# Kernel tuning notes

Measured on AMD Instinct MI355X. Metric: run time of the kernel, lower is better.

Reference implementation:

```python
import jax, jax.numpy as jnp
import numpy as np

D = 1024      # d_model
H = 16        # nhead
HD = D // H   # head_dim = 64
R = HD        # rotary_dim (default = head_dim)
N, T = 2, 2048
W_LEFT, W_RIGHT = 127, 128  # attn_window
ROPE_BASE = 10000.0


def _rope(x, cos, sin):
    # x: [N, T, H, HD]; cos/sin: [1, T, 1, R//2]; non-interleaved (rotate-half)
    x1 = x[..., : R // 2]
    x2 = x[..., R // 2 : R]
    rot = jnp.concatenate([x1 * cos - x2 * sin, x2 * cos + x1 * sin], axis=-1)
    if R < x.shape[-1]:
        rot = jnp.concatenate([rot, x[..., R:]], axis=-1)
    return rot


def setup_inputs() -> dict:
    key = jax.random.key(0)
    k1, k2, k3, k4 = jax.random.split(key, 4)
    x = jax.random.normal(k1, (N, T, D), dtype=jnp.float32)
    w_qkv = jax.random.normal(k2, (3 * D, D), dtype=jnp.float32) * 0.02
    w_out = jax.random.normal(k3, (D, D), dtype=jnp.float32) * 0.02
    b_out = jax.random.normal(k4, (D,), dtype=jnp.float32) * 0.02
    return {"x": x, "w_qkv": w_qkv, "w_out": w_out, "b_out": b_out}


def reference(x, w_qkv, w_out, b_out):
    n, t, _ = x.shape
    qkv = (x @ w_qkv.T).reshape(n, t, 3, H, HD)
    q, k, v = qkv[:, :, 0], qkv[:, :, 1], qkv[:, :, 2]  # [N, T, H, HD]

    # Rotary embedding (flash-attn RotaryEmbedding, interleaved=False)
    pos = jnp.arange(t, dtype=jnp.float32)
    inv_freq = 1.0 / (ROPE_BASE ** (jnp.arange(0, R, 2, dtype=jnp.float32) / R))
    freqs = pos[:, None] * inv_freq[None, :]          # [T, R//2]
    cos = jnp.cos(freqs)[None, :, None, :]
    sin = jnp.sin(freqs)[None, :, None, :]
    q = _rope(q, cos, sin)
    k = _rope(k, cos, sin)

    # Sliding-window band mask: keep j in [i - W_LEFT, i + W_RIGHT]
    i = jnp.arange(t)[:, None]
    j = jnp.arange(t)[None, :]
    band = (j >= i - W_LEFT) & (j <= i + W_RIGHT)      # [T, T] bool
    bias = jnp.where(band, 0.0, -jnp.inf).astype(x.dtype)

    scale = np.float32(1.0 / np.sqrt(HD))
    scores = jnp.einsum('nthd,nshd->nhts', q, k) * scale + bias  # [N, H, T, T]
    probs = jax.nn.softmax(scores, axis=-1)
    attn = jnp.einsum('nhts,nshd->nthd', probs, v).reshape(n, t, D)
    return attn @ w_out.T + b_out
```

## Files before the change

kernel.cpp:

```cpp
#include <hip/hip_runtime.h>
#include <math.h>

#define D_MODEL 1024
#define N_HEADS 16
#define HEAD_DIM 64
#define BATCH 2
#define SEQ 2048
#define WIN_L 127
#define WIN_R 128

typedef float f32x4 __attribute__((ext_vector_type(4)));
typedef __bf16 bf16x8 __attribute__((ext_vector_type(8)));
typedef unsigned short ushort8_t __attribute__((ext_vector_type(8)));

typedef const __attribute__((address_space(1))) void* gptr_t;
typedef __attribute__((address_space(3))) void* lptr_t;

__device__ __forceinline__ unsigned short f2bf(float v) {
    unsigned u = __float_as_uint(v);
    unsigned r = (u + 0x7FFF + ((u >> 16) & 1)) >> 16;
    return (unsigned short)r;
}

#define NX_ELEM (4096 * 1024)
#define NW_ELEM (3072 * 1024)
#define NO_ELEM (1024 * 1024)
#define NTOT_ELEM (NX_ELEM + NW_ELEM + NO_ELEM)
#define TAB_ELEM (SEQ * 32)

__global__ __launch_bounds__(256)
void cvt_all(const float* __restrict__ x, const float* __restrict__ wq,
             const float* __restrict__ wo, unsigned short* __restrict__ xb,
             unsigned short* __restrict__ wqb, unsigned short* __restrict__ wob,
             float2* __restrict__ ctab)
{
    int i = (blockIdx.x * 256 + threadIdx.x) * 4;
    if (i < NTOT_ELEM) {
        const float* src;
        unsigned short* dst;
        int off;
        if (i < NX_ELEM)                 { src = x;  dst = xb;  off = i; }
        else if (i < NX_ELEM + NW_ELEM)  { src = wq; dst = wqb; off = i - NX_ELEM; }
        else                             { src = wo; dst = wob; off = i - NX_ELEM - NW_ELEM; }
        float4 f = *(const float4*)(src + off);
        ushort4 o;
        o.x = f2bf(f.x); o.y = f2bf(f.y); o.z = f2bf(f.z); o.w = f2bf(f.w);
        *(ushort4*)(dst + off) = o;
    } else {
        int e0 = i - NTOT_ELEM;
#pragma unroll
        for (int e = 0; e < 4; ++e) {
            const int idx = e0 + e;
            const int t = idx >> 5;
            const int f = idx & 31;
            const float invf = exp2f(-(float)f * 0.41524101186092f);
            const float ang = (float)t * invf;
            ctab[idx] = make_float2(cosf(ang), sinf(ang));
        }
    }
}

__global__ __launch_bounds__(256, 3)
void gemm_qkv(const unsigned short* __restrict__ A,
              const unsigned short* __restrict__ B,
              unsigned short* __restrict__ qb,
              unsigned short* __restrict__ kb,
              unsigned short* __restrict__ vbT,
              const float2* __restrict__ ctab,
              int M, int N, int K)
{
    __shared__ __attribute__((aligned(16))) unsigned short U[17408];
    unsigned short* Al0 = U;
    unsigned short* Bl0 = U + 4096;
    unsigned short* Al1 = U + 8192;
    unsigned short* Bl1 = U + 12288;

    const int tid  = threadIdx.x;
    const int wave = tid >> 6;
    const int lane = tid & 63;
    const int m0 = blockIdx.y * 128;
    const int n0 = blockIdx.x * 128;

    const int wm = (wave >> 1) * 64;
    const int wn = (wave & 1) * 64;
    const int quad = lane >> 4;
    const int l16  = lane & 15;

    const int srow = lane >> 2;
    const int scol = (lane & 3) * 8;

    f32x4 acc[4][4] = {};

    for (int k0 = 0; k0 < K; k0 += 64) {
        __syncthreads();
#pragma unroll
        for (int l = 0; l < 2; ++l) {
            const int r = l * 64 + wave * 16 + srow;
            const unsigned short* gA = A + (size_t)(m0 + r) * K + k0 + scol;
            const unsigned short* gB = B + (size_t)(n0 + r) * K + k0 + scol;
            __builtin_amdgcn_global_load_lds((gptr_t)gA,        (lptr_t)&Al0[r * 32 + scol], 16, 0, 0);
            __builtin_amdgcn_global_load_lds((gptr_t)gB,        (lptr_t)&Bl0[r * 32 + scol], 16, 0, 0);
            __builtin_amdgcn_global_load_lds((gptr_t)(gA + 32), (lptr_t)&Al1[r * 32 + scol], 16, 0, 0);
            __builtin_amdgcn_global_load_lds((gptr_t)(gB + 32), (lptr_t)&Bl1[r * 32 + scol], 16, 0, 0);
        }
        __syncthreads();

#pragma unroll
        for (int kh = 0; kh < 2; ++kh) {
            const unsigned short* Ap = kh ? Al1 : Al0;
            const unsigned short* Bp = kh ? Bl1 : Bl0;
            bf16x8 af[4], bf[4];
#pragma unroll
            for (int i = 0; i < 4; ++i)
                af[i] = *(const bf16x8*)&Ap[(wm + i * 16 + l16) * 32 + quad * 8];
#pragma unroll
            for (int j = 0; j < 4; ++j)
                bf[j] = *(const bf16x8*)&Bp[(wn + j * 16 + l16) * 32 + quad * 8];
#pragma unroll
            for (int i = 0; i < 4; ++i)
#pragma unroll
                for (int j = 0; j < 4; ++j)
                    acc[i][j] = __builtin_amdgcn_mfma_f32_16x16x32_bf16(af[i], bf[j], acc[i][j], 0, 0, 0);
        }
    }

    __syncthreads();

    const int which = (n0 >> 10);
    unsigned short* Tw = U + wave * 4352;

    if (which != 2) {
#pragma unroll
        for (int i = 0; i < 4; ++i) {
            const int tb = (m0 + wm + i * 16 + quad * 4) & 2047;
#pragma unroll
            for (int jp = 0; jp < 2; ++jp)
#pragma unroll
                for (int r = 0; r < 4; ++r) {
                    const float2 cs = ctab[(tb + r) * 32 + jp * 16 + l16];
                    float x1 = acc[i][jp][r], x2 = acc[i][jp + 2][r];
                    acc[i][jp][r]     = x1 * cs.x - x2 * cs.y;
                    acc[i][jp + 2][r] = x2 * cs.x + x1 * cs.y;
                }
        }
#pragma unroll
        for (int i = 0; i < 4; ++i)
#pragma unroll
            for (int j = 0; j < 4; ++j)
#pragma unroll
                for (int r = 0; r < 4; ++r)
                    Tw[(i * 16 + quad * 4 + r) * 68 + j * 16 + l16] = f2bf(acc[i][j][r]);
    } else {
#pragma unroll
        for (int i = 0; i < 4; ++i)
#pragma unroll
            for (int j = 0; j < 4; ++j) {
                ushort4 pv;
                pv.x = f2bf(acc[i][j][0]); pv.y = f2bf(acc[i][j][1]);
                pv.z = f2bf(acc[i][j][2]); pv.w = f2bf(acc[i][j][3]);
                *(ushort4*)&Tw[(j * 16 + l16) * 68 + i * 16 + quad * 4] = pv;
            }
    }

    {
        const int h   = ((n0 + wn) >> 6) & 15;
        const int nb  = (m0 + wm) >> 11;
        const int tw0 = (m0 + wm) & 2047;
        const int lr8 = lane >> 3;
        const int lc8 = (lane & 7) * 8;
        if (which != 2) {
            unsigned short* dst = (which == 0 ? qb : kb);
            unsigned short* gb = dst + (((size_t)nb * 16 + h) * SEQ + tw0) * 64;
#pragma unroll
            for (int c = 0; c < 8; ++c) {
                const int row = c * 8 + lr8;
                ushort4 lo = *(const ushort4*)&Tw[row * 68 + lc8];
                ushort4 hi = *(const ushort4*)&Tw[row * 68 + lc8 + 4];
                ushort8_t v8 = {lo.x, lo.y, lo.z, lo.w, hi.x, hi.y, hi.z, hi.w};
                *(ushort8_t*)&gb[row * 64 + lc8] = v8;
            }
        } else {
            unsigned short* gb = vbT + ((size_t)nb * 16 + h) * 64 * SEQ + tw0;
#pragma unroll
            for (int c = 0; c < 8; ++c) {
                const int drow = c * 8 + lr8;
                ushort4 lo = *(const ushort4*)&Tw[drow * 68 + lc8];
                ushort4 hi = *(const ushort4*)&Tw[drow * 68 + lc8 + 4];
                ushort8_t v8 = {lo.x, lo.y, lo.z, lo.w, hi.x, hi.y, hi.z, hi.w};
                *(ushort8_t*)&gb[(size_t)drow * SEQ + lc8] = v8;
            }
        }
    }
}

__global__ __launch_bounds__(256, 4)
void gemm_out(const unsigned short* __restrict__ A,
              const unsigned short* __restrict__ B,
              const float* __restrict__ bias, float* __restrict__ C,
              int M, int N, int K)
{
    __shared__ __attribute__((aligned(16))) unsigned short Al0[64 * 32];
    __shared__ __attribute__((aligned(16))) unsigned short Al1[64 * 32];
    __shared__ __attribute__((aligned(16))) unsigned short Bl0[128 * 32];
    __shared__ __attribute__((aligned(16))) unsigned short Bl1[128 * 32];

    const int tid  = threadIdx.x;
    const int wave = tid >> 6;
    const int lane = tid & 63;
    const int m0 = blockIdx.y * 64;
    const int n0 = blockIdx.x * 128;

    const int wm = (wave >> 1) * 32;
    const int wn = (wave & 1) * 64;
    const int quad = lane >> 4;
    const int l16  = lane & 15;

    const int srow = lane >> 2;
    const int scol = (lane & 3) * 8;

    f32x4 acc[2][4] = {};

    for (int k0 = 0; k0 < K; k0 += 64) {
        __syncthreads();
        {
            const int r = wave * 16 + srow;
            const unsigned short* gA = A + (size_t)(m0 + r) * K + k0 + scol;
            __builtin_amdgcn_global_load_lds((gptr_t)gA,        (lptr_t)&Al0[r * 32 + scol], 16, 0, 0);
            __builtin_amdgcn_global_load_lds((gptr_t)(gA + 32), (lptr_t)&Al1[r * 32 + scol], 16, 0, 0);
#pragma unroll
            for (int l = 0; l < 2; ++l) {
                const int rb = l * 64 + wave * 16 + srow;
                const unsigned short* gB = B + (size_t)(n0 + rb) * K + k0 + scol;
                __builtin_amdgcn_global_load_lds((gptr_t)gB,        (lptr_t)&Bl0[rb * 32 + scol], 16, 0, 0);
                __builtin_amdgcn_global_load_lds((gptr_t)(gB + 32), (lptr_t)&Bl1[rb * 32 + scol], 16, 0, 0);
            }
        }
        __syncthreads();

#pragma unroll
        for (int kh = 0; kh < 2; ++kh) {
            const unsigned short* Ap = kh ? Al1 : Al0;
            const unsigned short* Bp = kh ? Bl1 : Bl0;
            bf16x8 af[2], bf[4];
#pragma unroll
            for (int i = 0; i < 2; ++i)
                af[i] = *(const bf16x8*)&Ap[(wm + i * 16 + l16) * 32 + quad * 8];
#pragma unroll
            for (int j = 0; j < 4; ++j)
                bf[j] = *(const bf16x8*)&Bp[(wn + j * 16 + l16) * 32 + quad * 8];
#pragma unroll
            for (int i = 0; i < 2; ++i)
#pragma unroll
                for (int j = 0; j < 4; ++j)
                    acc[i][j] = __builtin_amdgcn_mfma_f32_16x16x32_bf16(af[i], bf[j], acc[i][j], 0, 0, 0);
        }
    }

#pragma unroll
    for (int i = 0; i < 2; ++i) {
        const int row_base = m0 + wm + i * 16 + quad * 4;
#pragma unroll
        for (int j = 0; j < 4; ++j) {
            const int col = n0 + wn + j * 16 + l16;
            const float bv = bias[col];
#pragma unroll
            for (int r = 0; r < 4; ++r)
                C[(size_t)(row_base + r) * N + col] = acc[i][j][r] + bv;
        }
    }
}

__global__ __launch_bounds__(256, 3)
void attn_mfma(const unsigned short* __restrict__ qb,
               const unsigned short* __restrict__ kb,
               const unsigned short* __restrict__ vbT,
               unsigned short* __restrict__ attnb)
{
    __shared__ __attribute__((aligned(16))) unsigned short Pl[4][2][16 * 40];

    const int tid  = threadIdx.x;
    const int w    = tid >> 6;
    const int lane = tid & 63;
    const int quad = lane >> 4;
    const int l16  = lane & 15;

    const int t0 = blockIdx.x * 64;
    const int h  = blockIdx.y;
    const int nB = blockIdx.z;
    const int nh = nB * 16 + h;

    const int tw  = t0 + w * 16;
    const int klo = max(0, tw - WIN_L) & ~31;
    const int khi = min(SEQ, tw + 16 + WIN_R);
    const int nchunk = (khi - klo + 31) >> 5;

    const unsigned short* qrow = qb + ((size_t)nh * SEQ + tw + l16) * 64;
    bf16x8 aq0 = *(const bf16x8*)(qrow + quad * 8);
    bf16x8 aq1 = *(const bf16x8*)(qrow + 32 + quad * 8);

    const unsigned short* kbase = kb + (size_t)nh * SEQ * 64;
    const unsigned short* vbase = vbT + (size_t)nh * 64 * SEQ;

    const int trow = tw + quad * 4;

    f32x4 oacc[4] = {};
    float sm[4] = {0.f, 0.f, 0.f, 0.f};

    bf16x8 kA0, kA1, kB0, kB1;
    {
        const int keyA = klo + 2 * l16;
        const unsigned short* kpA = kbase + (size_t)min(keyA, SEQ - 1) * 64;
        const unsigned short* kpB = kbase + (size_t)min(keyA + 1, SEQ - 1) * 64;
        kA0 = *(const bf16x8*)(kpA + quad * 8);
        kA1 = *(const bf16x8*)(kpA + 32 + quad * 8);
        kB0 = *(const bf16x8*)(kpB + quad * 8);
        kB1 = *(const bf16x8*)(kpB + 32 + quad * 8);
    }

    for (int kc = 0; kc < nchunk; ++kc) {
        const int s0 = klo + kc * 32;
        const int keyA = s0 + 2 * l16;
        const int keyB = keyA + 1;

        bf16x8 vf[4];
        {
            const int vcol = s0 + quad * 8;
#pragma unroll
            for (int j = 0; j < 4; ++j)
                vf[j] = *(const bf16x8*)(vbase + (size_t)(j * 16 + l16) * SEQ + vcol);
        }

        bf16x8 nA0 = kA0, nA1 = kA1, nB0 = kB0, nB1 = kB1;
        if (kc + 1 < nchunk) {
            const int kyA = s0 + 32 + 2 * l16;
            const unsigned short* kpA = kbase + (size_t)min(kyA, SEQ - 1) * 64;
            const unsigned short* kpB = kbase + (size_t)min(kyA + 1, SEQ - 1) * 64;
            nA0 = *(const bf16x8*)(kpA + quad * 8);
            nA1 = *(const bf16x8*)(kpA + 32 + quad * 8);
            nB0 = *(const bf16x8*)(kpB + quad * 8);
            nB1 = *(const bf16x8*)(kpB + 32 + quad * 8);
        }

        f32x4 sa = {0.f, 0.f, 0.f, 0.f};
        f32x4 sb = {0.f, 0.f, 0.f, 0.f};
        __builtin_amdgcn_s_setprio(1);
        sa = __builtin_amdgcn_mfma_f32_16x16x32_bf16(aq0, kA0, sa, 0, 0, 0);
        sa = __builtin_amdgcn_mfma_f32_16x16x32_bf16(aq1, kA1, sa, 0, 0, 0);
        sb = __builtin_amdgcn_mfma_f32_16x16x32_bf16(aq0, kB0, sb, 0, 0, 0);
        sb = __builtin_amdgcn_mfma_f32_16x16x32_bf16(aq1, kB1, sb, 0, 0, 0);
        __builtin_amdgcn_s_setprio(0);

        unsigned short* Pc = &Pl[w][kc & 1][0];
#pragma unroll
        for (int r = 0; r < 4; ++r) {
            const int t = trow + r;
            const bool vA = (keyA < khi) && (keyA >= t - WIN_L) && (keyA <= t + WIN_R);
            const bool vB = (keyB < khi) && (keyB >= t - WIN_L) && (keyB <= t + WIN_R);
            float p0 = vA ? exp2f(sa[r] * 0.18033688011f) : 0.f;
            float p1 = vB ? exp2f(sb[r] * 0.18033688011f) : 0.f;
            sm[r] += p0 + p1;
            unsigned pk = (unsigned)f2bf(p0) | ((unsigned)f2bf(p1) << 16);
            *(unsigned*)&Pc[(quad * 4 + r) * 40 + 2 * l16] = pk;
        }

        bf16x8 pf = *(const bf16x8*)&Pc[l16 * 40 + quad * 8];
        __builtin_amdgcn_s_setprio(1);
#pragma unroll
        for (int j = 0; j < 4; ++j)
            oacc[j] = __builtin_amdgcn_mfma_f32_16x16x32_bf16(pf, vf[j], oacc[j], 0, 0, 0);
        __builtin_amdgcn_s_setprio(0);

        kA0 = nA0; kA1 = nA1; kB0 = nB0; kB1 = nB1;
    }

#pragma unroll
    for (int r = 0; r < 4; ++r) {
#pragma unroll
        for (int o = 8; o >= 1; o >>= 1) sm[r] += __shfl_xor(sm[r], o, 64);
        sm[r] = 1.0f / sm[r];
    }

#pragma unroll
    for (int j = 0; j < 4; ++j)
#pragma unroll
        for (int r = 0; r < 4; ++r) {
            const int t = trow + r;
            attnb[((size_t)(nB * SEQ + t)) * D_MODEL + h * 64 + j * 16 + l16] =
                f2bf(oacc[j][r] * sm[r]);
        }
}

extern "C" void kernel_launch(void* const* d_in, const int* in_sizes, int n_in,
                              void* d_out, int out_size, void* d_ws, size_t ws_size,
                              hipStream_t stream)
{
    (void)in_sizes; (void)n_in; (void)out_size; (void)ws_size;
    const float* x     = (const float*)d_in[0];
    const float* w_qkv = (const float*)d_in[1];
    const float* w_out = (const float*)d_in[2];
    const float* b_out = (const float*)d_in[3];
    float* out = (float*)d_out;

    const int M = BATCH * SEQ;

    unsigned short* qb  = (unsigned short*)d_ws;
    unsigned short* kb  = qb  + (size_t)4194304;
    unsigned short* vbT = kb  + (size_t)4194304;
    unsigned short* wob = vbT + (size_t)4194304;
    unsigned short* xb  = wob + (size_t)1048576;
    unsigned short* wqb = xb  + (size_t)4194304;
    float2* ctab = (float2*)(wqb + (size_t)4194304);
    unsigned short* attnb = xb;

    dim3 blk(256);

    cvt_all<<<dim3((NTOT_ELEM + TAB_ELEM * 4) / 4 / 256), blk, 0, stream>>>(
        x, w_qkv, w_out, xb, wqb, wob, ctab);

    gemm_qkv<<<dim3(3 * D_MODEL / 128, M / 128), blk, 0, stream>>>(
        xb, wqb, qb, kb, vbT, ctab, M, 3 * D_MODEL, D_MODEL);

    attn_mfma<<<dim3(SEQ / 64, N_HEADS, BATCH), blk, 0, stream>>>(qb, kb, vbT, attnb);

    gemm_out<<<dim3(D_MODEL / 128, M / 64), blk, 0, stream>>>(
        attnb, wob, b_out, out, M, D_MODEL, D_MODEL);
}
```

Baseline: 174.4 us.

## Transpose attention MFMAs to keep P in registers and stage V in LDS

Swaps the MFMA operand order so the score output lands in the layout needed as the B operand of the PV product. This removes the per-chunk LDS round trip for P. The V tile covering the block's whole key window is loaded once into shared memory with global_load_lds, replacing the per-wave global V loads. The row-sum reduction now shuffles across quads, and output is written with vectorized 4-element stores. The cost is a larger LDS footprint (about 41KB), which may limit occupancy under launch_bounds(256,3), plus an upfront barrier before compute.

```diff
diff --git a/kernel.cpp b/kernel.cpp
--- a/kernel.cpp
+++ b/kernel.cpp
@@ -276,7 +276,7 @@
                const unsigned short* __restrict__ vbT,
                unsigned short* __restrict__ attnb)
 {
-    __shared__ __attribute__((aligned(16))) unsigned short Pl[4][2][16 * 40];
+    __shared__ __attribute__((aligned(16))) unsigned short Vl[64 * 328];
 
     const int tid  = threadIdx.x;
     const int w    = tid >> 6;
@@ -289,22 +289,40 @@
     const int nB = blockIdx.z;
     const int nh = nB * 16 + h;
 
+    const int klo_b = max(0, t0 - WIN_L) & ~31;
+
+    {
+        const unsigned short* vbase = vbT + (size_t)nh * 64 * SEQ;
+#pragma unroll
+        for (int k = 0; k < 11; ++k) {
+            const int s = k * 256 + tid;
+            if (s < 64 * 41) {
+                const int row = s / 41;
+                const int seg = s - row * 41;
+                const int tsrc = min(klo_b + seg * 8, SEQ - 8);
+                __builtin_amdgcn_global_load_lds(
+                    (gptr_t)(vbase + (size_t)row * SEQ + tsrc),
+                    (lptr_t)&Vl[s * 8], 16, 0, 0);
+            }
+        }
+    }
+    __syncthreads();
+
     const int tw  = t0 + w * 16;
     const int klo = max(0, tw - WIN_L) & ~31;
     const int khi = min(SEQ, tw + 16 + WIN_R);
     const int nchunk = (khi - klo + 31) >> 5;
 
-    const unsigned short* qrow = qb + ((size_t)nh * SEQ + tw + l16) * 64;
+    const int tq = tw + l16;
+
+    const unsigned short* qrow = qb + ((size_t)nh * SEQ + tq) * 64;
     bf16x8 aq0 = *(const bf16x8*)(qrow + quad * 8);
     bf16x8 aq1 = *(const bf16x8*)(qrow + 32 + quad * 8);
 
     const unsigned short* kbase = kb + (size_t)nh * SEQ * 64;
-    const unsigned short* vbase = vbT + (size_t)nh * 64 * SEQ;
-
-    const int trow = tw + quad * 4;
 
     f32x4 oacc[4] = {};
-    float sm[4] = {0.f, 0.f, 0.f, 0.f};
+    float sm = 0.f;
 
     bf16x8 kA0, kA1, kB0, kB1;
     {
@@ -319,16 +337,6 @@
 
     for (int kc = 0; kc < nchunk; ++kc) {
         const int s0 = klo + kc * 32;
-        const int keyA = s0 + 2 * l16;
-        const int keyB = keyA + 1;
-
-        bf16x8 vf[4];
-        {
-            const int vcol = s0 + quad * 8;
-#pragma unroll
-            for (int j = 0; j < 4; ++j)
-                vf[j] = *(const bf16x8*)(vbase + (size_t)(j * 16 + l16) * SEQ + vcol);
-        }
 
         bf16x8 nA0 = kA0, nA1 = kA1, nB0 = kB0, nB1 = kB1;
         if (kc + 1 < nchunk) {
@@ -344,50 +352,53 @@
         f32x4 sa = {0.f, 0.f, 0.f, 0.f};
         f32x4 sb = {0.f, 0.f, 0.f, 0.f};
         __builtin_amdgcn_s_setprio(1);
-        sa = __builtin_amdgcn_mfma_f32_16x16x32_bf16(aq0, kA0, sa, 0, 0, 0);
-        sa = __builtin_amdgcn_mfma_f32_16x16x32_bf16(aq1, kA1, sa, 0, 0, 0);
-        sb = __builtin_amdgcn_mfma_f32_16x16x32_bf16(aq0, kB0, sb, 0, 0, 0);
-        sb = __builtin_amdgcn_mfma_f32_16x16x32_bf16(aq1, kB1, sb, 0, 0, 0);
+        sa = __builtin_amdgcn_mfma_f32_16x16x32_bf16(kA0, aq0, sa, 0, 0, 0);
+        sa = __builtin_amdgcn_mfma_f32_16x16x32_bf16(kA1, aq1, sa, 0, 0, 0);
+        sb = __builtin_amdgcn_mfma_f32_16x16x32_bf16(kB0, aq0, sb, 0, 0, 0);
+        sb = __builtin_amdgcn_mfma_f32_16x16x32_bf16(kB1, aq1, sb, 0, 0, 0);
         __builtin_amdgcn_s_setprio(0);
 
-        unsigned short* Pc = &Pl[w][kc & 1][0];
+        ushort8_t pk;
 #pragma unroll
         for (int r = 0; r < 4; ++r) {
-            const int t = trow + r;
-            const bool vA = (keyA < khi) && (keyA >= t - WIN_L) && (keyA <= t + WIN_R);
-            const bool vB = (keyB < khi) && (keyB >= t - WIN_L) && (keyB <= t + WIN_R);
+            const int ka = s0 + 8 * quad + 2 * r;
+            const int kb2 = ka + 1;
+            const bool vA = (ka  < khi) && (ka  >= tq - WIN_L) && (ka  <= tq + WIN_R);
+            const bool vB = (kb2 < khi) && (kb2 >= tq - WIN_L) && (kb2 <= tq + WIN_R);
             float p0 = vA ? exp2f(sa[r] * 0.18033688011f) : 0.f;
             float p1 = vB ? exp2f(sb[r] * 0.18033688011f) : 0.f;
-            sm[r] += p0 + p1;
-            unsigned pk = (unsigned)f2bf(p0) | ((unsigned)f2bf(p1) << 16);
-            *(unsigned*)&Pc[(quad * 4 + r) * 40 + 2 * l16] = pk;
-        }
-
-        bf16x8 pf = *(const bf16x8*)&Pc[l16 * 40 + quad * 8];
+            sm += p0 + p1;
+            pk[2 * r]     = f2bf(p0);
+            pk[2 * r + 1] = f2bf(p1);
+        }
+        bf16x8 pf = *(bf16x8*)&pk;
+
+        const int rel = s0 - klo_b + quad * 8;
         __builtin_amdgcn_s_setprio(1);
 #pragma unroll
-        for (int j = 0; j < 4; ++j)
-            oacc[j] = __builtin_amdgcn_mfma_f32_16x16x32_bf16(pf, vf[j], oacc[j], 0, 0, 0);
+        for (int j = 0; j < 4; ++j) {
+            bf16x8 vf = *(const bf16x8*)&Vl[(j * 16 + l16) * 328 + rel];
+            oacc[j] = __builtin_amdgcn_mfma_f32_16x16x32_bf16(vf, pf, oacc[j], 0, 0, 0);
+        }
         __builtin_amdgcn_s_setprio(0);
 
         kA0 = nA0; kA1 = nA1; kB0 = nB0; kB1 = nB1;
     }
 
-#pragma unroll
-    for (int r = 0; r < 4; ++r) {
-#pragma unroll
-        for (int o = 8; o >= 1; o >>= 1) sm[r] += __shfl_xor(sm[r], o, 64);
-        sm[r] = 1.0f / sm[r];
-    }
-
-#pragma unroll
-    for (int j = 0; j < 4; ++j)
-#pragma unroll
-        for (int r = 0; r < 4; ++r) {
-            const int t = trow + r;
-            attnb[((size_t)(nB * SEQ + t)) * D_MODEL + h * 64 + j * 16 + l16] =
-                f2bf(oacc[j][r] * sm[r]);
-        }
+    sm += __shfl_xor(sm, 16, 64);
+    sm += __shfl_xor(sm, 32, 64);
+    const float inv = 1.0f / sm;
+
+    unsigned short* orow = attnb + ((size_t)(nB * SEQ + tq)) * D_MODEL + h * 64;
+#pragma unroll
+    for (int j = 0; j < 4; ++j) {
+        ushort4 o4;
+        o4.x = f2bf(oacc[j][0] * inv);
+        o4.y = f2bf(oacc[j][1] * inv);
+        o4.z = f2bf(oacc[j][2] * inv);
+        o4.w = f2bf(oacc[j][3] * inv);
+        *(ushort4*)&orow[j * 16 + quad * 4] = o4;
+    }
 }
 
 extern "C" void kernel_launch(void* const* d_in, const int* in_sizes, int n_in,
```

Result: faster. 164.9 us (-5.5%).
